# Kernel optimization log

Hardware: AMD Instinct MI355X
Metric: run time of the kernel (lower is better)

## Reference

```python
import jax, jax.numpy as jnp
import numpy as np

D_MODEL = 1024
N_HEADS = 16
HEAD_DIM = D_MODEL // N_HEADS


def setup_inputs() -> dict:
    key = jax.random.key(0)
    k1, k2, k3 = jax.random.split(key, 3)
    x = jax.random.normal(k1, (4, 2048, D_MODEL), dtype=jnp.float32)
    # per-head qkv Linear (bias=False): torch weight [3*head_dim, d_model];
    # store transposed and stacked over heads: [H, d_model, 3*head_dim]
    w_qkv = jax.random.normal(k2, (N_HEADS, D_MODEL, 3 * HEAD_DIM), dtype=jnp.float32) * (1.0 / np.sqrt(D_MODEL))
    # output Linear (bias=False), stored transposed: [d_model, d_model]
    w_out = jax.random.normal(k3, (D_MODEL, D_MODEL), dtype=jnp.float32) * (1.0 / np.sqrt(D_MODEL))
    return {"x": x, "w_qkv": w_qkv, "w_out": w_out}


def reference(x, w_qkv, w_out):
    hd = HEAD_DIM
    # all heads' qkv in one contraction: [B, H, S, 3*hd]
    qkv = jnp.einsum("bsd,hde->bhse", x, w_qkv)
    q, k, v = qkv[..., :hd], qkv[..., hd:2 * hd], qkv[..., 2 * hd:]
    scale = 1.0 / hd  # NOTE: original scales by 1/dk, not 1/sqrt(dk)
    scores = jnp.einsum("bhqe,bhke->bhqk", q, k) * scale
    attn = jax.nn.softmax(scores, axis=-1)
    z = jnp.einsum("bhqk,bhke->bhqe", attn, v)  # [B, H, S, hd]
    # concat heads along feature dim (head order = list order)
    b, h, s, _ = z.shape
    z = jnp.transpose(z, (0, 2, 1, 3)).reshape(b, s, h * hd)
    return z @ w_out
```

## Files before the change

### kernel.cpp

```cpp
#include <hip/hip_runtime.h>
#include <hip/hip_bf16.h>

typedef unsigned short u16;
typedef __attribute__((ext_vector_type(4))) float f32x4;
typedef __attribute__((ext_vector_type(16))) float f32x16;
typedef __attribute__((ext_vector_type(8))) short s16x8;
typedef __attribute__((ext_vector_type(4))) unsigned short u16x4;

static __device__ __forceinline__ u16 f32_to_bf16(float f) {
    union { float f; unsigned u; } v; v.f = f;
    unsigned r = v.u + 0x7FFF + ((v.u >> 16) & 1);
    return (u16)(r >> 16);
}

static __device__ __forceinline__ unsigned cvt_pk_bf16(float lo, float hi) {
    unsigned r;
    asm("v_cvt_pk_bf16_f32 %0, %1, %2" : "=v"(r) : "v"(lo), "v"(hi));
    return r;
}

static __device__ __forceinline__ void pswap2(unsigned &a, unsigned &b) {
#if defined(__has_builtin) && __has_builtin(__builtin_amdgcn_permlane32_swap)
    auto r = __builtin_amdgcn_permlane32_swap(a, b, false, false);
    a = r[0]; b = r[1];
#else
    asm volatile("v_permlane32_swap_b32 %0, %1" : "+v"(a), "+v"(b));
#endif
}

static __device__ __forceinline__ float fexp2(float x) {
#if defined(__has_builtin) && __has_builtin(__builtin_amdgcn_exp2f)
    return __builtin_amdgcn_exp2f(x);
#else
    return exp2f(x);
#endif
}

#define GLOAD_LDS16(gptr, lptr) \
    __builtin_amdgcn_global_load_lds((const __attribute__((address_space(1))) void*)(gptr), \
                                     (__attribute__((address_space(3))) void*)(lptr), 16, 0, 0)


__global__ void cvt_f32_bf16(const float* __restrict__ in, u16* __restrict__ out, int n) {
    int i = (blockIdx.x * 256 + threadIdx.x) * 4;
    if (i + 3 < n) {
        f32x4 v = *(const f32x4*)(in + i);
        u16x4 o;
        o.x = f32_to_bf16(v.x); o.y = f32_to_bf16(v.y);
        o.z = f32_to_bf16(v.z); o.w = f32_to_bf16(v.w);
        *(u16x4*)(out + i) = o;
    }
}

__global__ void cvt_wqkvT(const float* __restrict__ w, u16* __restrict__ wt) {
    int tid = blockIdx.x * 256 + threadIdx.x;
    int k = tid & 1023, n = tid >> 10;
    int h = n / 192, e = n - h * 192;
    wt[tid] = f32_to_bf16(w[(h * 1024 + k) * 192 + e]);
}

__global__ void cvt_woutT(const float* __restrict__ w, u16* __restrict__ wt) {
    int tid = blockIdx.x * 256 + threadIdx.x;
    int k = tid & 1023, n = tid >> 10;
    wt[tid] = f32_to_bf16(w[k * 1024 + n]);
}


template <int EPI>
__global__ __launch_bounds__(256, 4)
void gemm_bt(const u16* __restrict__ A, const u16* __restrict__ B,
             float* __restrict__ Cf, u16* __restrict__ Qb, u16* __restrict__ Kb,
             u16* __restrict__ Vt, int M, int N, int K) {
    __shared__ __align__(16) u16 lA[2][128 * 32];
    __shared__ __align__(16) u16 lB[2][128 * 32];

    const int t = threadIdx.x;
    const int lane = t & 63;
    const int wave = t >> 6;
    const int wr = wave >> 1, wc = wave & 1;
    const int l15 = lane & 15, g = lane >> 4;

    const int nwg = gridDim.x;
    const int cpx = nwg >> 3;
    const int orig = blockIdx.x;
    const int logical = (orig & 7) * cpx + (orig >> 3);

    const int nbx = N >> 7;
    const int bx = logical % nbx, by = logical / nbx;
    const int bm = by << 7, bn = bx << 7;

    f32x4 acc[4][4] = {};

    const int sr0 = t >> 2;
    const int ss  = t & 3;

    const u16* Abase = A + (size_t)bm * K;
    const u16* Bbase = B + (size_t)bn * K;

#define GSTAGE(buf, kt) do { \
    _Pragma("unroll") \
    for (int c = 0; c < 2; ++c) { \
        int r = sr0 + 64 * c; \
        int cl = ss ^ (r & 3); \
        GLOAD_LDS16(Abase + (size_t)r * K + (kt) + cl * 8, &lA[buf][(r * 4 + ss) * 8]); \
        GLOAD_LDS16(Bbase + (size_t)r * K + (kt) + cl * 8, &lB[buf][(r * 4 + ss) * 8]); \
    } } while (0)

    GSTAGE(0, 0);

    const int NT = K >> 5;
    for (int ti = 0; ti < NT; ++ti) {
        __syncthreads();
        if (ti + 1 < NT) GSTAGE((ti + 1) & 1, (ti + 1) << 5);

        const u16* Ac = lA[ti & 1];
        const u16* Bc = lB[ti & 1];
        s16x8 a[4], b[4];
#pragma unroll
        for (int i = 0; i < 4; ++i) {
            int r = wr * 64 + i * 16 + l15;
            int sl = g ^ (r & 3);
            a[i] = *(const s16x8*)&Ac[(r * 4 + sl) * 8];
        }
#pragma unroll
        for (int j = 0; j < 4; ++j) {
            int r = wc * 64 + j * 16 + l15;
            int sl = g ^ (r & 3);
            b[j] = *(const s16x8*)&Bc[(r * 4 + sl) * 8];
        }
#pragma unroll
        for (int i = 0; i < 4; ++i)
#pragma unroll
            for (int j = 0; j < 4; ++j)
                acc[i][j] = __builtin_amdgcn_mfma_f32_16x16x32_bf16(b[j], a[i], acc[i][j], 0, 0, 0);
    }
#undef GSTAGE

    if constexpr (EPI == 0) {
#pragma unroll
        for (int i = 0; i < 4; ++i) {
            int m = bm + wr * 64 + i * 16 + l15;
#pragma unroll
            for (int j = 0; j < 4; ++j) {
                int n0 = bn + wc * 64 + j * 16 + g * 4;
                *(f32x4*)&Cf[(size_t)m * N + n0] = acc[i][j];
            }
        }
    } else {
        const float qscale = 0.022542110013890054f;
#pragma unroll
        for (int j = 0; j < 4; ++j) {
            int n0 = bn + wc * 64 + j * 16 + g * 4;
            int h = n0 / 192;
            int e0 = n0 - h * 192;
#pragma unroll
            for (int i = 0; i < 4; ++i) {
                int m = bm + wr * 64 + i * 16 + l15;
                int bb = m >> 11, s = m & 2047;
                int bh = bb * 16 + h;
                if (e0 < 64) {
                    u16x4 q;
#pragma unroll
                    for (int r = 0; r < 4; ++r) q[r] = f32_to_bf16(acc[i][j][r] * qscale);
                    *(u16x4*)&Qb[((size_t)bh * 2048 + s) * 64 + e0] = q;
                } else if (e0 < 128) {
                    u16x4 kk;
#pragma unroll
                    for (int r = 0; r < 4; ++r) kk[r] = f32_to_bf16(acc[i][j][r]);
                    *(u16x4*)&Kb[((size_t)bh * 2048 + s) * 64 + (e0 - 64)] = kk;
                } else {
#pragma unroll
                    for (int r = 0; r < 4; ++r)
                        Vt[((size_t)bh * 64 + (e0 - 128 + r)) * 2048 + s] = f32_to_bf16(acc[i][j][r]);
                }
            }
        }
    }
}

__global__ __launch_bounds__(512, 4)
void attn32(const u16* __restrict__ Qb, const u16* __restrict__ Kb,
            const u16* __restrict__ Vt, u16* __restrict__ Zb) {
    __shared__ __align__(16) u16 lK[2][128 * 64];
    __shared__ __align__(16) u16 lV[2][64 * 128];

    const int t = threadIdx.x;
    const int lane = t & 63;
    const int w = t >> 6;
    const int l31 = lane & 31, hi = lane >> 5;
    const int r7 = l31 & 7;

    const int orig = blockIdx.x;
    const int logical = (orig & 7) * 64 + (orig >> 3);
    const int bh = logical >> 3;
    const int qt = logical & 7;
    const int q0 = qt * 256 + w * 32;

    const u16* Kbh = Kb + (size_t)bh * 2048 * 64;
    const u16* Vbh = Vt + (size_t)bh * 64 * 2048;

    const u16* Qp = Qb + ((size_t)bh * 2048 + q0 + l31) * 64 + hi * 8;
    s16x8 qf[4];
#pragma unroll
    for (int kd = 0; kd < 4; ++kd) qf[kd] = *(const s16x8*)(Qp + kd * 16);

    s16x8 ones;
#pragma unroll
    for (int i = 0; i < 8; ++i) ones[i] = (short)0x3F80;

    f32x16 o0 = {}, o1 = {}, ol = {};

#define STAGE(buf, kvn) do { \
    _Pragma("unroll") \
    for (int j = 0; j < 2; ++j) { \
        int kr = w * 16 + j * 8 + (lane >> 3); \
        GLOAD_LDS16(Kbh + (size_t)((kvn) + kr) * 64 + ((lane & 7) ^ (lane >> 3)) * 8, \
                    &lK[buf][w * 1024 + j * 512 + lane * 8]); \
        int vr = w * 8 + j * 4 + (lane >> 4); \
        int vcl = (lane & 15) ^ (j * 4 + (lane >> 4)); \
        GLOAD_LDS16(Vbh + (size_t)vr * 2048 + (kvn) + vcl * 8, \
                    &lV[buf][w * 1024 + j * 512 + lane * 8]); \
    } } while (0)

    STAGE(0, 0);
    __syncthreads();

#pragma unroll 2
    for (int ti = 0; ti < 16; ++ti) {
        const int cur = ti & 1;
        const int kvn = ((ti + 1) & 15) * 128;

        STAGE(cur ^ 1, kvn);

        const u16* Kc = &lK[cur][0];
        const u16* Vc = &lV[cur][0];

#pragma unroll
        for (int hs = 0; hs < 2; ++hs) {
            f32x16 p0 = {}, p1 = {};
            __builtin_amdgcn_s_setprio(1);
#pragma unroll
            for (int kd = 0; kd < 4; ++kd) {
                int cs = ((2 * kd + hi) ^ r7) * 8;
                s16x8 kf0 = *(const s16x8*)&Kc[(hs * 64 + l31) * 64 + cs];
                p0 = __builtin_amdgcn_mfma_f32_32x32x16_bf16(kf0, qf[kd], p0, 0, 0, 0);
                s16x8 kf1 = *(const s16x8*)&Kc[(hs * 64 + l31 + 32) * 64 + cs];
                p1 = __builtin_amdgcn_mfma_f32_32x32x16_bf16(kf1, qf[kd], p1, 0, 0, 0);
            }
            __builtin_amdgcn_s_setprio(0);

#pragma unroll
            for (int r = 0; r < 16; ++r) { p0[r] = fexp2(p0[r]); p1[r] = fexp2(p1[r]); }

            union { unsigned u[8]; s16x8 v[2]; } pa0, pa1;
            {
                unsigned c0 = cvt_pk_bf16(p0[0],  p0[1]);
                unsigned c1 = cvt_pk_bf16(p0[2],  p0[3]);
                unsigned c2 = cvt_pk_bf16(p0[4],  p0[5]);
                unsigned c3 = cvt_pk_bf16(p0[6],  p0[7]);
                unsigned c4 = cvt_pk_bf16(p0[8],  p0[9]);
                unsigned c5 = cvt_pk_bf16(p0[10], p0[11]);
                unsigned c6 = cvt_pk_bf16(p0[12], p0[13]);
                unsigned c7 = cvt_pk_bf16(p0[14], p0[15]);
                pswap2(c0, c2); pswap2(c1, c3);
                pswap2(c4, c6); pswap2(c5, c7);
                pa0.u[0] = c0; pa0.u[1] = c1; pa0.u[2] = c2; pa0.u[3] = c3;
                pa0.u[4] = c4; pa0.u[5] = c5; pa0.u[6] = c6; pa0.u[7] = c7;
            }
            __builtin_amdgcn_s_setprio(1);
#pragma unroll
            for (int ks = 0; ks < 2; ++ks) {
                s16x8 pav = pa0.v[ks];
                int cs = ((hs * 8 + ks * 2 + hi) ^ r7) * 8;
                s16x8 vf0 = *(const s16x8*)&Vc[l31 * 128 + cs];
                o0 = __builtin_amdgcn_mfma_f32_32x32x16_bf16(pav, vf0, o0, 0, 0, 0);
                s16x8 vf1 = *(const s16x8*)&Vc[(l31 + 32) * 128 + cs];
                o1 = __builtin_amdgcn_mfma_f32_32x32x16_bf16(pav, vf1, o1, 0, 0, 0);
                ol = __builtin_amdgcn_mfma_f32_32x32x16_bf16(pav, ones, ol, 0, 0, 0);
            }
            __builtin_amdgcn_s_setprio(0);

            {
                unsigned c0 = cvt_pk_bf16(p1[0],  p1[1]);
                unsigned c1 = cvt_pk_bf16(p1[2],  p1[3]);
                unsigned c2 = cvt_pk_bf16(p1[4],  p1[5]);
                unsigned c3 = cvt_pk_bf16(p1[6],  p1[7]);
                unsigned c4 = cvt_pk_bf16(p1[8],  p1[9]);
                unsigned c5 = cvt_pk_bf16(p1[10], p1[11]);
                unsigned c6 = cvt_pk_bf16(p1[12], p1[13]);
                unsigned c7 = cvt_pk_bf16(p1[14], p1[15]);
                pswap2(c0, c2); pswap2(c1, c3);
                pswap2(c4, c6); pswap2(c5, c7);
                pa1.u[0] = c0; pa1.u[1] = c1; pa1.u[2] = c2; pa1.u[3] = c3;
                pa1.u[4] = c4; pa1.u[5] = c5; pa1.u[6] = c6; pa1.u[7] = c7;
            }
            __builtin_amdgcn_s_setprio(1);
#pragma unroll
            for (int ks = 0; ks < 2; ++ks) {
                s16x8 pav = pa1.v[ks];
                int cs = ((hs * 8 + 4 + ks * 2 + hi) ^ r7) * 8;
                s16x8 vf0 = *(const s16x8*)&Vc[l31 * 128 + cs];
                o0 = __builtin_amdgcn_mfma_f32_32x32x16_bf16(pav, vf0, o0, 0, 0, 0);
                s16x8 vf1 = *(const s16x8*)&Vc[(l31 + 32) * 128 + cs];
                o1 = __builtin_amdgcn_mfma_f32_32x32x16_bf16(pav, vf1, o1, 0, 0, 0);
                ol = __builtin_amdgcn_mfma_f32_32x32x16_bf16(pav, ones, ol, 0, 0, 0);
            }
            __builtin_amdgcn_s_setprio(0);
        }

        __syncthreads();
    }
#undef STAGE

    const int bq = bh >> 4, hq = bh & 15;
#pragma unroll
    for (int r = 0; r < 16; ++r) {
        int qrow = (r & 3) + 8 * (r >> 2) + 4 * hi;
        float inv = 1.0f / ol[r];
        size_t rowbase = ((size_t)(bq * 2048 + q0 + qrow)) * 1024 + hq * 64 + l31;
        Zb[rowbase]      = f32_to_bf16(o0[r] * inv);
        Zb[rowbase + 32] = f32_to_bf16(o1[r] * inv);
    }
}


extern "C" void kernel_launch(void* const* d_in, const int* in_sizes, int n_in,
                              void* d_out, int out_size, void* d_ws, size_t ws_size,
                              hipStream_t stream) {
    const float* x     = (const float*)d_in[0];
    const float* w_qkv = (const float*)d_in[1];
    const float* w_out = (const float*)d_in[2];
    float* out = (float*)d_out;

    char* ws = (char*)d_ws;
    u16* xb  = (u16*)ws; ws += (size_t)8192 * 1024 * 2;
    u16* wqT = (u16*)ws; ws += (size_t)3072 * 1024 * 2;
    u16* woT = (u16*)ws; ws += (size_t)1024 * 1024 * 2;
    u16* Qb  = (u16*)ws; ws += (size_t)64 * 2048 * 64 * 2;
    u16* Kb  = (u16*)ws; ws += (size_t)64 * 2048 * 64 * 2;
    u16* Vt  = (u16*)ws; ws += (size_t)64 * 2048 * 64 * 2;
    u16* Zb  = (u16*)ws; ws += (size_t)8192 * 1024 * 2;

    cvt_f32_bf16<<<dim3(8192), dim3(256), 0, stream>>>(x, xb, 8192 * 1024);
    cvt_wqkvT<<<dim3(12288), dim3(256), 0, stream>>>(w_qkv, wqT);
    cvt_woutT<<<dim3(4096), dim3(256), 0, stream>>>(w_out, woT);

    gemm_bt<1><<<dim3(64 * 24), dim3(256), 0, stream>>>(xb, wqT, nullptr, Qb, Kb, Vt,
                                                        8192, 3072, 1024);
    attn32<<<dim3(512), dim3(512), 0, stream>>>(Qb, Kb, Vt, Zb);
    gemm_bt<0><<<dim3(64 * 8), dim3(256), 0, stream>>>(Zb, woT, out, nullptr, nullptr, nullptr,
                                                       8192, 1024, 1024);
}
```

Before: 212.4 us.

## Restructure attention into 4-wave blocks with 64-key triple-buffered LDS pipeline

The attention kernel moves from 512-thread blocks covering 256 queries to 256-thread blocks covering 128 queries, with twice as many blocks. Keys and values are staged in 64-key tiles across a three-slot LDS ring, and the wait before each barrier is a partial vmcnt wait, so two tiles can be in flight while one is computed. The goal is more loads overlapping compute and better occupancy or scheduling flexibility. In exchange there are more barriers per key sweep, and each K/V tile is reloaded by twice as many blocks.

New measurement: 222.7 us. +4.8%, slower.

```diff
diff --git a/kernel.cpp b/kernel.cpp
--- a/kernel.cpp
+++ b/kernel.cpp
@@ -178,11 +178,11 @@
     }
 }
 
-__global__ __launch_bounds__(512, 4)
+__global__ __launch_bounds__(256, 3)
 void attn32(const u16* __restrict__ Qb, const u16* __restrict__ Kb,
             const u16* __restrict__ Vt, u16* __restrict__ Zb) {
-    __shared__ __align__(16) u16 lK[2][128 * 64];
-    __shared__ __align__(16) u16 lV[2][64 * 128];
+    __shared__ __align__(16) u16 lK[3 * 64 * 64];
+    __shared__ __align__(16) u16 lV[3 * 64 * 64];
 
     const int t = threadIdx.x;
     const int lane = t & 63;
@@ -191,10 +191,10 @@
     const int r7 = l31 & 7;
 
     const int orig = blockIdx.x;
-    const int logical = (orig & 7) * 64 + (orig >> 3);
-    const int bh = logical >> 3;
-    const int qt = logical & 7;
-    const int q0 = qt * 256 + w * 32;
+    const int logical = (orig & 7) * 128 + (orig >> 3);
+    const int bh = logical >> 4;
+    const int qt = logical & 15;
+    const int q0 = qt * 128 + w * 32;
 
     const u16* Kbh = Kb + (size_t)bh * 2048 * 64;
     const u16* Vbh = Vt + (size_t)bh * 64 * 2048;
@@ -210,105 +210,99 @@
 
     f32x16 o0 = {}, o1 = {}, ol = {};
 
-#define STAGE(buf, kvn) do { \
+#define STAGE(bb, kvn) do { \
     _Pragma("unroll") \
     for (int j = 0; j < 2; ++j) { \
-        int kr = w * 16 + j * 8 + (lane >> 3); \
-        GLOAD_LDS16(Kbh + (size_t)((kvn) + kr) * 64 + ((lane & 7) ^ (lane >> 3)) * 8, \
-                    &lK[buf][w * 1024 + j * 512 + lane * 8]); \
-        int vr = w * 8 + j * 4 + (lane >> 4); \
-        int vcl = (lane & 15) ^ (j * 4 + (lane >> 4)); \
-        GLOAD_LDS16(Vbh + (size_t)vr * 2048 + (kvn) + vcl * 8, \
-                    &lV[buf][w * 1024 + j * 512 + lane * 8]); \
+        int r_ = w * 16 + j * 8 + (lane >> 3); \
+        int c_ = ((lane & 7) ^ (lane >> 3)) * 8; \
+        GLOAD_LDS16(Kbh + (size_t)((kvn) + r_) * 64 + c_, \
+                    &lK[(bb) + w * 1024 + j * 512 + lane * 8]); \
+        GLOAD_LDS16(Vbh + (size_t)r_ * 2048 + (kvn) + c_, \
+                    &lV[(bb) + w * 1024 + j * 512 + lane * 8]); \
     } } while (0)
 
     STAGE(0, 0);
-    __syncthreads();
-
-#pragma unroll 2
-    for (int ti = 0; ti < 16; ++ti) {
-        const int cur = ti & 1;
-        const int kvn = ((ti + 1) & 15) * 128;
-
-        STAGE(cur ^ 1, kvn);
-
-        const u16* Kc = &lK[cur][0];
-        const u16* Vc = &lV[cur][0];
-
-#pragma unroll
-        for (int hs = 0; hs < 2; ++hs) {
-            f32x16 p0 = {}, p1 = {};
-            __builtin_amdgcn_s_setprio(1);
-#pragma unroll
-            for (int kd = 0; kd < 4; ++kd) {
-                int cs = ((2 * kd + hi) ^ r7) * 8;
-                s16x8 kf0 = *(const s16x8*)&Kc[(hs * 64 + l31) * 64 + cs];
-                p0 = __builtin_amdgcn_mfma_f32_32x32x16_bf16(kf0, qf[kd], p0, 0, 0, 0);
-                s16x8 kf1 = *(const s16x8*)&Kc[(hs * 64 + l31 + 32) * 64 + cs];
-                p1 = __builtin_amdgcn_mfma_f32_32x32x16_bf16(kf1, qf[kd], p1, 0, 0, 0);
-            }
-            __builtin_amdgcn_s_setprio(0);
-
-#pragma unroll
-            for (int r = 0; r < 16; ++r) { p0[r] = fexp2(p0[r]); p1[r] = fexp2(p1[r]); }
-
-            union { unsigned u[8]; s16x8 v[2]; } pa0, pa1;
-            {
-                unsigned c0 = cvt_pk_bf16(p0[0],  p0[1]);
-                unsigned c1 = cvt_pk_bf16(p0[2],  p0[3]);
-                unsigned c2 = cvt_pk_bf16(p0[4],  p0[5]);
-                unsigned c3 = cvt_pk_bf16(p0[6],  p0[7]);
-                unsigned c4 = cvt_pk_bf16(p0[8],  p0[9]);
-                unsigned c5 = cvt_pk_bf16(p0[10], p0[11]);
-                unsigned c6 = cvt_pk_bf16(p0[12], p0[13]);
-                unsigned c7 = cvt_pk_bf16(p0[14], p0[15]);
-                pswap2(c0, c2); pswap2(c1, c3);
-                pswap2(c4, c6); pswap2(c5, c7);
-                pa0.u[0] = c0; pa0.u[1] = c1; pa0.u[2] = c2; pa0.u[3] = c3;
-                pa0.u[4] = c4; pa0.u[5] = c5; pa0.u[6] = c6; pa0.u[7] = c7;
-            }
-            __builtin_amdgcn_s_setprio(1);
-#pragma unroll
-            for (int ks = 0; ks < 2; ++ks) {
-                s16x8 pav = pa0.v[ks];
-                int cs = ((hs * 8 + ks * 2 + hi) ^ r7) * 8;
-                s16x8 vf0 = *(const s16x8*)&Vc[l31 * 128 + cs];
-                o0 = __builtin_amdgcn_mfma_f32_32x32x16_bf16(pav, vf0, o0, 0, 0, 0);
-                s16x8 vf1 = *(const s16x8*)&Vc[(l31 + 32) * 128 + cs];
-                o1 = __builtin_amdgcn_mfma_f32_32x32x16_bf16(pav, vf1, o1, 0, 0, 0);
-                ol = __builtin_amdgcn_mfma_f32_32x32x16_bf16(pav, ones, ol, 0, 0, 0);
-            }
-            __builtin_amdgcn_s_setprio(0);
-
-            {
-                unsigned c0 = cvt_pk_bf16(p1[0],  p1[1]);
-                unsigned c1 = cvt_pk_bf16(p1[2],  p1[3]);
-                unsigned c2 = cvt_pk_bf16(p1[4],  p1[5]);
-                unsigned c3 = cvt_pk_bf16(p1[6],  p1[7]);
-                unsigned c4 = cvt_pk_bf16(p1[8],  p1[9]);
-                unsigned c5 = cvt_pk_bf16(p1[10], p1[11]);
-                unsigned c6 = cvt_pk_bf16(p1[12], p1[13]);
-                unsigned c7 = cvt_pk_bf16(p1[14], p1[15]);
-                pswap2(c0, c2); pswap2(c1, c3);
-                pswap2(c4, c6); pswap2(c5, c7);
-                pa1.u[0] = c0; pa1.u[1] = c1; pa1.u[2] = c2; pa1.u[3] = c3;
-                pa1.u[4] = c4; pa1.u[5] = c5; pa1.u[6] = c6; pa1.u[7] = c7;
-            }
-            __builtin_amdgcn_s_setprio(1);
-#pragma unroll
-            for (int ks = 0; ks < 2; ++ks) {
-                s16x8 pav = pa1.v[ks];
-                int cs = ((hs * 8 + 4 + ks * 2 + hi) ^ r7) * 8;
-                s16x8 vf0 = *(const s16x8*)&Vc[l31 * 128 + cs];
-                o0 = __builtin_amdgcn_mfma_f32_32x32x16_bf16(pav, vf0, o0, 0, 0, 0);
-                s16x8 vf1 = *(const s16x8*)&Vc[(l31 + 32) * 128 + cs];
-                o1 = __builtin_amdgcn_mfma_f32_32x32x16_bf16(pav, vf1, o1, 0, 0, 0);
-                ol = __builtin_amdgcn_mfma_f32_32x32x16_bf16(pav, ones, ol, 0, 0, 0);
-            }
-            __builtin_amdgcn_s_setprio(0);
-        }
-
-        __syncthreads();
+    STAGE(4096, 64);
+    asm volatile("s_waitcnt vmcnt(4)" ::: "memory");
+    __builtin_amdgcn_s_barrier();
+    __builtin_amdgcn_sched_barrier(0);
+
+    int i0 = 0, i1 = 4096, i2 = 8192;
+
+    for (int ti = 0; ti < 32; ++ti) {
+        const bool more = (ti < 30);
+        if (more) STAGE(i2, (ti + 2) << 6);
+
+        const u16* Kc = &lK[i0];
+        const u16* Vc = &lV[i0];
+
+        f32x16 p0 = {}, p1 = {};
+        __builtin_amdgcn_s_setprio(1);
+#pragma unroll
+        for (int kd = 0; kd < 4; ++kd) {
+            int cs = ((2 * kd + hi) ^ r7) * 8;
+            s16x8 kf0 = *(const s16x8*)&Kc[l31 * 64 + cs];
+            p0 = __builtin_amdgcn_mfma_f32_32x32x16_bf16(kf0, qf[kd], p0, 0, 0, 0);
+            s16x8 kf1 = *(const s16x8*)&Kc[(l31 + 32) * 64 + cs];
+            p1 = __builtin_amdgcn_mfma_f32_32x32x16_bf16(kf1, qf[kd], p1, 0, 0, 0);
+        }
+        __builtin_amdgcn_s_setprio(0);
+
+#pragma unroll
+        for (int r = 0; r < 16; ++r) { p0[r] = fexp2(p0[r]); p1[r] = fexp2(p1[r]); }
+
+        union { unsigned u[8]; s16x8 v[2]; } pa0, pa1;
+        {
+            unsigned c0 = cvt_pk_bf16(p0[0],  p0[1]);
+            unsigned c1 = cvt_pk_bf16(p0[2],  p0[3]);
+            unsigned c2 = cvt_pk_bf16(p0[4],  p0[5]);
+            unsigned c3 = cvt_pk_bf16(p0[6],  p0[7]);
+            unsigned c4 = cvt_pk_bf16(p0[8],  p0[9]);
+            unsigned c5 = cvt_pk_bf16(p0[10], p0[11]);
+            unsigned c6 = cvt_pk_bf16(p0[12], p0[13]);
+            unsigned c7 = cvt_pk_bf16(p0[14], p0[15]);
+            pswap2(c0, c2); pswap2(c1, c3);
+            pswap2(c4, c6); pswap2(c5, c7);
+            pa0.u[0] = c0; pa0.u[1] = c1; pa0.u[2] = c2; pa0.u[3] = c3;
+            pa0.u[4] = c4; pa0.u[5] = c5; pa0.u[6] = c6; pa0.u[7] = c7;
+        }
+        {
+            unsigned c0 = cvt_pk_bf16(p1[0],  p1[1]);
+            unsigned c1 = cvt_pk_bf16(p1[2],  p1[3]);
+            unsigned c2 = cvt_pk_bf16(p1[4],  p1[5]);
+            unsigned c3 = cvt_pk_bf16(p1[6],  p1[7]);
+            unsigned c4 = cvt_pk_bf16(p1[8],  p1[9]);
+            unsigned c5 = cvt_pk_bf16(p1[10], p1[11]);
+            unsigned c6 = cvt_pk_bf16(p1[12], p1[13]);
+            unsigned c7 = cvt_pk_bf16(p1[14], p1[15]);
+            pswap2(c0, c2); pswap2(c1, c3);
+            pswap2(c4, c6); pswap2(c5, c7);
+            pa1.u[0] = c0; pa1.u[1] = c1; pa1.u[2] = c2; pa1.u[3] = c3;
+            pa1.u[4] = c4; pa1.u[5] = c5; pa1.u[6] = c6; pa1.u[7] = c7;
+        }
+
+        __builtin_amdgcn_s_setprio(1);
+#pragma unroll
+        for (int ks = 0; ks < 4; ++ks) {
+            s16x8 pav = (ks < 2) ? pa0.v[ks] : pa1.v[ks - 2];
+            int cs = ((ks * 2 + hi) ^ r7) * 8;
+            s16x8 vf0 = *(const s16x8*)&Vc[l31 * 64 + cs];
+            o0 = __builtin_amdgcn_mfma_f32_32x32x16_bf16(pav, vf0, o0, 0, 0, 0);
+            s16x8 vf1 = *(const s16x8*)&Vc[(l31 + 32) * 64 + cs];
+            o1 = __builtin_amdgcn_mfma_f32_32x32x16_bf16(pav, vf1, o1, 0, 0, 0);
+            ol = __builtin_amdgcn_mfma_f32_32x32x16_bf16(pav, ones, ol, 0, 0, 0);
+        }
+        __builtin_amdgcn_s_setprio(0);
+
+        if (more) {
+            asm volatile("s_waitcnt vmcnt(4)" ::: "memory");
+        } else {
+            asm volatile("s_waitcnt vmcnt(0)" ::: "memory");
+        }
+        __builtin_amdgcn_s_barrier();
+        __builtin_amdgcn_sched_barrier(0);
+
+        int tmp = i0; i0 = i1; i1 = i2; i2 = tmp;
     }
 #undef STAGE
 
@@ -347,7 +341,7 @@
 
     gemm_bt<1><<<dim3(64 * 24), dim3(256), 0, stream>>>(xb, wqT, nullptr, Qb, Kb, Vt,
                                                         8192, 3072, 1024);
-    attn32<<<dim3(512), dim3(512), 0, stream>>>(Qb, Kb, Vt, Zb);
+    attn32<<<dim3(1024), dim3(256), 0, stream>>>(Qb, Kb, Vt, Zb);
     gemm_bt<0><<<dim3(64 * 8), dim3(256), 0, stream>>>(Zb, woT, out, nullptr, nullptr, nullptr,
                                                        8192, 1024, 1024);
 }
```
